# Kernel optimization log

Measured on AMD Instinct MI355X. Metric: run time of the kernel, lower is better.

Reference implementation:

```python
import jax, jax.numpy as jnp
import numpy as np

H = 16
D_MODEL = 1024
D_K = D_MODEL // H
B, S = 2, 2048


def setup_inputs() -> dict:
    key = jax.random.key(0)
    ks = jax.random.split(key, 11)
    scale = 1.0 / np.sqrt(D_MODEL)
    inp = {
        "query": jax.random.normal(ks[0], (B, S, D_MODEL), jnp.float32),
        "key": jax.random.normal(ks[1], (B, S, D_MODEL), jnp.float32),
        "value": jax.random.normal(ks[2], (B, S, D_MODEL), jnp.float32),
        # four nn.Linear(d_model, d_model): Wq, Wk, Wv, Wo (torch convention: y = x @ W.T + b)
        "Wq": jax.random.uniform(ks[3], (D_MODEL, D_MODEL), jnp.float32, -scale, scale),
        "bq": jax.random.uniform(ks[4], (D_MODEL,), jnp.float32, -scale, scale),
        "Wk": jax.random.uniform(ks[5], (D_MODEL, D_MODEL), jnp.float32, -scale, scale),
        "bk": jax.random.uniform(ks[6], (D_MODEL,), jnp.float32, -scale, scale),
        "Wv": jax.random.uniform(ks[7], (D_MODEL, D_MODEL), jnp.float32, -scale, scale),
        "bv": jax.random.uniform(ks[8], (D_MODEL,), jnp.float32, -scale, scale),
        "Wo": jax.random.uniform(ks[9], (D_MODEL, D_MODEL), jnp.float32, -scale, scale),
        "bo": jax.random.uniform(ks[10], (D_MODEL,), jnp.float32, -scale, scale),
    }
    return inp


def _split_heads(x):
    # [B, S, D] -> [B, H, S, d_k]
    b, s, _ = x.shape
    return x.reshape(b, s, H, D_K).transpose(0, 2, 1, 3)


def reference(query, key, value, Wq, bq, Wk, bk, Wv, bv, Wo, bo):
    q = _split_heads(query @ Wq.T + bq)
    k = _split_heads(key @ Wk.T + bk)
    v = _split_heads(value @ Wv.T + bv)
    # scaled dot-product attention (dropout omitted: reference is eval-mode)
    scores = jnp.einsum("bhqd,bhkd->bhqk", q, k) / np.sqrt(D_K).astype(np.float32)
    p = jax.nn.softmax(scores, axis=-1)
    x = jnp.einsum("bhqk,bhkd->bhqd", p, v)
    x = x.transpose(0, 2, 1, 3).reshape(query.shape[0], -1, H * D_K)
    return x @ Wo.T + bo
```

## Files before the change

kernel.cpp:

```cpp
#include <hip/hip_runtime.h>

typedef unsigned short u16;
typedef unsigned int u32;
typedef __attribute__((ext_vector_type(8))) short short8;
typedef __attribute__((ext_vector_type(4))) float floatx4;
typedef __attribute__((ext_vector_type(4))) unsigned short ushortx4;
typedef __attribute__((ext_vector_type(2))) unsigned int uint2v;

#define DEV static __device__ __forceinline__

DEV float bf2f(u16 u) { union { unsigned u; float f; } v; v.u = ((unsigned)u) << 16; return v.f; }
DEV u16 f2bf(float f) {
  union { float f; unsigned u; } v; v.f = f;
  return (u16)((v.u + 0x7FFFu + ((v.u >> 16) & 1u)) >> 16);
}
DEV u32 pkbf(float a, float b) {
  union { float f; u32 u; } x, y; x.f = a; y.f = b;
  return __builtin_amdgcn_perm(y.u + 0x8000u, x.u + 0x8000u, 0x07060302u);
}
DEV float fexp2(float x) { return __builtin_amdgcn_exp2f(x); }

#define GLDS(g, l) __builtin_amdgcn_global_load_lds( \
    (const __attribute__((address_space(1))) void*)(g), \
    (__attribute__((address_space(3))) void*)(l), 16, 0, 0)

struct CvtArg {
  const float* src[11];
  u16* dst[11];
  int cum[12];
};

__global__ void convert(CvtArg a) {
  const long base = ((long)blockIdx.x * 256 + threadIdx.x) * 4;
  if (base >= a.cum[11]) return;
  int s = 0;
  while (s < 10 && base >= a.cum[s + 1]) ++s;
  const long off = base - a.cum[s];
  const float* sp = a.src[s] + off;
  ushortx4 u;
#pragma unroll
  for (int r = 0; r < 4; ++r) u[r] = f2bf(sp[r]);
  *(ushortx4*)(a.dst[s] + off) = u;
}

struct GemmArg {
  const u16* x;
  const u16* w;
  const u16* bias;
  u16* dst;
  int mode;
};

__global__ __launch_bounds__(256, 2) void gemm_nt(GemmArg g0, GemmArg g1, GemmArg g2) {
  GemmArg g = (blockIdx.z == 0) ? g0 : ((blockIdx.z == 1) ? g1 : g2);
  __shared__ u16 As[128 * 32];
  __shared__ u16 Bs[128 * 32];
  const int tid = threadIdx.x, w = tid >> 6, l = tid & 63;
  const int l15 = l & 15, quad = l >> 4;
  const int bm = blockIdx.x, bn = blockIdx.y;
  const int wm = w >> 1, wn = w & 1;

  floatx4 acc[4][4];
#pragma unroll
  for (int i = 0; i < 4; ++i)
#pragma unroll
    for (int j = 0; j < 4; ++j) acc[i][j] = (floatx4){0.f, 0.f, 0.f, 0.f};

  const u16* xb = g.x + (long)(bm * 128 + w * 16 + (l >> 2)) * 1024 + (l & 3) * 8;
  const u16* wb = g.w + (long)(bn * 128 + w * 16 + (l >> 2)) * 1024 + (l & 3) * 8;
  u16* asb = &As[(w * 16) * 32];
  u16* bsb = &Bs[(w * 16) * 32];

  for (int kt = 0; kt < 32; ++kt) {
    const int k0 = kt * 32;
    __syncthreads();
#pragma unroll
    for (int p = 0; p < 2; ++p) {
      GLDS(xb + (long)p * 64 * 1024 + k0, asb + p * 64 * 32);
      GLDS(wb + (long)p * 64 * 1024 + k0, bsb + p * 64 * 32);
    }
    __syncthreads();
    short8 af[4], bfr[4];
#pragma unroll
    for (int mi = 0; mi < 4; ++mi)
      af[mi] = *(const short8*)&As[(wm * 64 + mi * 16 + l15) * 32 + quad * 8];
#pragma unroll
    for (int ni = 0; ni < 4; ++ni)
      bfr[ni] = *(const short8*)&Bs[(wn * 64 + ni * 16 + l15) * 32 + quad * 8];
#pragma unroll
    for (int mi = 0; mi < 4; ++mi)
#pragma unroll
      for (int ni = 0; ni < 4; ++ni)
        acc[mi][ni] = __builtin_amdgcn_mfma_f32_16x16x32_bf16(af[mi], bfr[ni], acc[mi][ni], 0, 0, 0);
  }

  float bv[4];
#pragma unroll
  for (int ni = 0; ni < 4; ++ni) bv[ni] = bf2f(g.bias[bn * 128 + wn * 64 + ni * 16 + l15]);

#pragma unroll
  for (int mi = 0; mi < 4; ++mi) {
    const int mbase = bm * 128 + wm * 64 + mi * 16 + quad * 4;
#pragma unroll
    for (int ni = 0; ni < 4; ++ni) {
      const int n = bn * 128 + wn * 64 + ni * 16 + l15;
      if (g.mode == 2) {
        const int b = mbase >> 11, s = mbase & 2047;
        const int h = n >> 6, d = n & 63;
        ushortx4 u;
#pragma unroll
        for (int r = 0; r < 4; ++r) u[r] = f2bf(acc[mi][ni][r] + bv[ni]);
        *(ushortx4*)&g.dst[((long)(b * 16 + h) * 64 + d) * 2048 + s] = u;
      } else if (g.mode == 3) {
        float* df = (float*)g.dst;
#pragma unroll
        for (int r = 0; r < 4; ++r)
          df[(long)(mbase + r) * 1024 + n] = acc[mi][ni][r] + bv[ni];
      } else {
        const float sc = (g.mode == 0) ? 0.18033688011f : 1.0f;
        const int h = n >> 6, d = n & 63;
#pragma unroll
        for (int r = 0; r < 4; ++r) {
          const int m = mbase + r, b = m >> 11, s = m & 2047;
          g.dst[((long)(b * 16 + h) * 2048 + s) * 64 + d] = f2bf((acc[mi][ni][r] + bv[ni]) * sc);
        }
      }
    }
  }
}

__global__ __launch_bounds__(256, 3) void attn_flash(const u16* __restrict__ Q,
                                                     const u16* __restrict__ K,
                                                     const u16* __restrict__ V,
                                                     u16* __restrict__ X) {
  __shared__ u16 Ks[64 * 72];
  __shared__ u16 Vs[64 * 72];
  __shared__ u16 Ps[4][32 * 72];
  __shared__ float denW[4][32];
  const int tid = threadIdx.x, w = tid >> 6, l = tid & 63;
  const int l15 = l & 15, quad = l >> 4;
  const int q0 = blockIdx.x * 128, bh = blockIdx.y;
  const u16* qp = Q + (long)bh * 2048 * 64;
  const u16* kp = K + (long)bh * 2048 * 64;
  const u16* vp = V + (long)bh * 2048 * 64;

  short8 qf[2][2];
#pragma unroll
  for (int nq = 0; nq < 2; ++nq)
#pragma unroll
    for (int kc = 0; kc < 2; ++kc)
      qf[nq][kc] = *(const short8*)(qp + (long)(q0 + w * 32 + nq * 16 + l15) * 64 + kc * 32 + quad * 8);

  floatx4 o[2][4];
#pragma unroll
  for (int mq = 0; mq < 2; ++mq)
#pragma unroll
    for (int nd = 0; nd < 4; ++nd) o[mq][nd] = (floatx4){0.f, 0.f, 0.f, 0.f};
  float den[2] = {0.f, 0.f};

  for (int kv0 = 0; kv0 < 2048; kv0 += 64) {
    __syncthreads();
#pragma unroll
    for (int i = 0; i < 2; ++i) {
      const int ci = i * 256 + tid;
      const int r = ci >> 3, c8 = ci & 7;
      short8 tk = *(const short8*)(kp + (long)(kv0 + r) * 64 + c8 * 8);
      short8 tv = *(const short8*)(vp + (long)r * 2048 + kv0 + c8 * 8);
      *(short8*)&Ks[r * 72 + c8 * 8] = tk;
      *(short8*)&Vs[r * 72 + c8 * 8] = tv;
    }
    __syncthreads();

#pragma unroll
    for (int mk = 0; mk < 4; ++mk) {
      short8 ak0 = *(const short8*)&Ks[(mk * 16 + l15) * 72 + quad * 8];
      short8 ak1 = *(const short8*)&Ks[(mk * 16 + l15) * 72 + 32 + quad * 8];
#pragma unroll
      for (int nq = 0; nq < 2; ++nq) {
        floatx4 st = (floatx4){0.f, 0.f, 0.f, 0.f};
        st = __builtin_amdgcn_mfma_f32_16x16x32_bf16(ak0, qf[nq][0], st, 0, 0, 0);
        st = __builtin_amdgcn_mfma_f32_16x16x32_bf16(ak1, qf[nq][1], st, 0, 0, 0);
        const float e0 = fexp2(st[0]), e1 = fexp2(st[1]);
        const float e2 = fexp2(st[2]), e3 = fexp2(st[3]);
        den[nq] += (e0 + e1) + (e2 + e3);
        uint2v pk = { pkbf(e0, e1), pkbf(e2, e3) };
        *(uint2v*)&Ps[w][(nq * 16 + l15) * 72 + mk * 16 + quad * 4] = pk;
      }
    }

#pragma unroll
    for (int kc = 0; kc < 2; ++kc) {
#pragma unroll
      for (int mq = 0; mq < 2; ++mq) {
        short8 ap = *(const short8*)&Ps[w][(mq * 16 + l15) * 72 + kc * 32 + quad * 8];
#pragma unroll
        for (int nd = 0; nd < 4; ++nd) {
          short8 bvf = *(const short8*)&Vs[(nd * 16 + l15) * 72 + kc * 32 + quad * 8];
          o[mq][nd] = __builtin_amdgcn_mfma_f32_16x16x32_bf16(ap, bvf, o[mq][nd], 0, 0, 0);
        }
      }
    }
  }

#pragma unroll
  for (int nq = 0; nq < 2; ++nq) {
    float d = den[nq];
    d += __shfl_xor(d, 16);
    d += __shfl_xor(d, 32);
    if (l < 16) denW[w][nq * 16 + l] = 1.0f / d;
  }

  const int b = bh >> 4, h = bh & 15;
#pragma unroll
  for (int mq = 0; mq < 2; ++mq) {
#pragma unroll
    for (int r = 0; r < 4; ++r) {
      const float rcp = denW[w][mq * 16 + quad * 4 + r];
      const int s = q0 + w * 32 + mq * 16 + quad * 4 + r;
      u16* xrow = X + ((long)(b * 2048 + s)) * 1024 + h * 64;
#pragma unroll
      for (int nd = 0; nd < 4; ++nd)
        xrow[nd * 16 + l15] = f2bf(o[mq][nd][r] * rcp);
    }
  }
}

extern "C" void kernel_launch(void* const* d_in, const int* in_sizes, int n_in,
                              void* d_out, int out_size, void* d_ws, size_t ws_size,
                              hipStream_t stream) {
  u16* ws = (u16*)d_ws;
  const size_t M1 = 1048576, M4 = 4194304;
  u16* NQ  = ws;
  u16* NK  = ws + M4;
  u16* NV  = ws + 2 * M4;
  u16* NWQ = ws + 3 * M4;
  u16* NWK = ws + 3 * M4 + M1;
  u16* NWV = ws + 3 * M4 + 2 * M1;
  u16* NWO = ws + 3 * M4 + 3 * M1;
  u16* NBQ = ws + 3 * M4 + 4 * M1;
  u16* NBK = NBQ + 1024;
  u16* NBV = NBQ + 2048;
  u16* NBO = NBQ + 3072;
  u16* Qb = ws + 16 * M1 + 8192;
  u16* Kb = Qb + M4;
  u16* Vb = Qb + 2 * M4;
  u16* Xb = NQ;

  CvtArg ca;
  u16* dsts[11] = {NQ, NK, NV, NWQ, NBQ, NWK, NBK, NWV, NBV, NWO, NBO};
  int sizes[11] = {(int)M4, (int)M4, (int)M4, (int)M1, 1024, (int)M1, 1024, (int)M1, 1024, (int)M1, 1024};
  int c = 0;
  for (int i = 0; i < 11; ++i) {
    ca.src[i] = (const float*)d_in[i];
    ca.dst[i] = dsts[i];
    ca.cum[i] = c;
    c += sizes[i];
  }
  ca.cum[11] = c;
  convert<<<(c / 4 + 255) / 256, 256, 0, stream>>>(ca);

  GemmArg gq{NQ, NWQ, NBQ, Qb, 0};
  GemmArg gk{NK, NWK, NBK, Kb, 1};
  GemmArg gv{NV, NWV, NBV, Vb, 2};
  gemm_nt<<<dim3(32, 8, 3), 256, 0, stream>>>(gq, gk, gv);

  attn_flash<<<dim3(16, 32), 256, 0, stream>>>(Qb, Kb, Vb, Xb);

  GemmArg go{Xb, NWO, NBO, (u16*)d_out, 3};
  gemm_nt<<<dim3(32, 8, 1), 256, 0, stream>>>(go, go, go);
}
```

Measured before the change: 240.3 us.

## Double-buffer K/V tiles in LDS with register prefetch in attention kernel

The attention kernel now keeps two LDS buffers for K and V and issues global loads for tile t+2 into registers while tile t is being computed. Those registers are written into the alternate buffer at the end of each iteration, which removes one barrier per iteration and hides global load latency. The PV loop is also reordered so each V fragment is loaded once and feeds both query sub-tiles. In exchange, LDS use and register pressure go up, and the occupancy hint drops from 3 to 2 blocks per SM.

```diff
diff --git a/kernel.cpp b/kernel.cpp
--- a/kernel.cpp
+++ b/kernel.cpp
@@ -129,12 +129,12 @@
   }
 }
 
-__global__ __launch_bounds__(256, 3) void attn_flash(const u16* __restrict__ Q,
+__global__ __launch_bounds__(256, 2) void attn_flash(const u16* __restrict__ Q,
                                                      const u16* __restrict__ K,
                                                      const u16* __restrict__ V,
                                                      u16* __restrict__ X) {
-  __shared__ u16 Ks[64 * 72];
-  __shared__ u16 Vs[64 * 72];
+  __shared__ u16 Ks[2][64 * 72];
+  __shared__ u16 Vs[2][64 * 72];
   __shared__ u16 Ps[4][32 * 72];
   __shared__ float denW[4][32];
   const int tid = threadIdx.x, w = tid >> 6, l = tid & 63;
@@ -144,6 +144,23 @@
   const u16* kp = K + (long)bh * 2048 * 64;
   const u16* vp = V + (long)bh * 2048 * 64;
 
+  const int r0 = tid >> 3, c0 = tid & 7;
+  const int r1 = (256 + tid) >> 3, c1 = tid & 7;
+
+#define ISSUE_LOADS(kv0) \
+    sk0 = *(const short8*)(kp + (long)((kv0) + r0) * 64 + c0 * 8); \
+    sv0 = *(const short8*)(vp + (long)r0 * 2048 + (kv0) + c0 * 8); \
+    sk1 = *(const short8*)(kp + (long)((kv0) + r1) * 64 + c1 * 8); \
+    sv1 = *(const short8*)(vp + (long)r1 * 2048 + (kv0) + c1 * 8);
+
+#define STORE_TILE(pb) \
+    *(short8*)&Ks[pb][r0 * 72 + c0 * 8] = sk0; \
+    *(short8*)&Vs[pb][r0 * 72 + c0 * 8] = sv0; \
+    *(short8*)&Ks[pb][r1 * 72 + c1 * 8] = sk1; \
+    *(short8*)&Vs[pb][r1 * 72 + c1 * 8] = sv1;
+
+  short8 sk0, sv0, sk1, sv1;
+
   short8 qf[2][2];
 #pragma unroll
   for (int nq = 0; nq < 2; ++nq)
@@ -158,23 +175,18 @@
     for (int nd = 0; nd < 4; ++nd) o[mq][nd] = (floatx4){0.f, 0.f, 0.f, 0.f};
   float den[2] = {0.f, 0.f};
 
-  for (int kv0 = 0; kv0 < 2048; kv0 += 64) {
-    __syncthreads();
-#pragma unroll
-    for (int i = 0; i < 2; ++i) {
-      const int ci = i * 256 + tid;
-      const int r = ci >> 3, c8 = ci & 7;
-      short8 tk = *(const short8*)(kp + (long)(kv0 + r) * 64 + c8 * 8);
-      short8 tv = *(const short8*)(vp + (long)r * 2048 + kv0 + c8 * 8);
-      *(short8*)&Ks[r * 72 + c8 * 8] = tk;
-      *(short8*)&Vs[r * 72 + c8 * 8] = tv;
-    }
-    __syncthreads();
+  ISSUE_LOADS(0)
+  STORE_TILE(0)
+  ISSUE_LOADS(64)
+  __syncthreads();
+
+  for (int t = 0; t < 32; ++t) {
+    const int p = t & 1;
 
 #pragma unroll
     for (int mk = 0; mk < 4; ++mk) {
-      short8 ak0 = *(const short8*)&Ks[(mk * 16 + l15) * 72 + quad * 8];
-      short8 ak1 = *(const short8*)&Ks[(mk * 16 + l15) * 72 + 32 + quad * 8];
+      short8 ak0 = *(const short8*)&Ks[p][(mk * 16 + l15) * 72 + quad * 8];
+      short8 ak1 = *(const short8*)&Ks[p][(mk * 16 + l15) * 72 + 32 + quad * 8];
 #pragma unroll
       for (int nq = 0; nq < 2; ++nq) {
         floatx4 st = (floatx4){0.f, 0.f, 0.f, 0.f};
@@ -190,16 +202,24 @@
 
 #pragma unroll
     for (int kc = 0; kc < 2; ++kc) {
-#pragma unroll
-      for (int mq = 0; mq < 2; ++mq) {
-        short8 ap = *(const short8*)&Ps[w][(mq * 16 + l15) * 72 + kc * 32 + quad * 8];
-#pragma unroll
-        for (int nd = 0; nd < 4; ++nd) {
-          short8 bvf = *(const short8*)&Vs[(nd * 16 + l15) * 72 + kc * 32 + quad * 8];
-          o[mq][nd] = __builtin_amdgcn_mfma_f32_16x16x32_bf16(ap, bvf, o[mq][nd], 0, 0, 0);
-        }
-      }
-    }
+      short8 ap0 = *(const short8*)&Ps[w][l15 * 72 + kc * 32 + quad * 8];
+      short8 ap1 = *(const short8*)&Ps[w][(16 + l15) * 72 + kc * 32 + quad * 8];
+#pragma unroll
+      for (int nd = 0; nd < 4; ++nd) {
+        short8 bvf = *(const short8*)&Vs[p][(nd * 16 + l15) * 72 + kc * 32 + quad * 8];
+        o[0][nd] = __builtin_amdgcn_mfma_f32_16x16x32_bf16(ap0, bvf, o[0][nd], 0, 0, 0);
+        o[1][nd] = __builtin_amdgcn_mfma_f32_16x16x32_bf16(ap1, bvf, o[1][nd], 0, 0, 0);
+      }
+    }
+
+    if (t < 31) {
+      STORE_TILE(p ^ 1)
+      if (t < 30) {
+        const int nxt = (t + 2) * 64;
+        ISSUE_LOADS(nxt)
+      }
+    }
+    __syncthreads();
   }
 
 #pragma unroll
```

After: 227.8 us. 5.2% less time.
